# Performance work log

Measured on AMD Instinct MI355X. Metric: run time of the kernel, lower is better.

## Reference

```python
import jax, jax.numpy as jnp
import numpy as np

B, S, IN_DIM, D_MODEL, H = 1, 4096, 512, 512, 8
DK = D_MODEL // H


def setup_inputs() -> dict:
    key = jax.random.key(0)
    ks = jax.random.split(key, 10)
    sc_in = 1.0 / np.sqrt(IN_DIM)
    sc_dm = 1.0 / np.sqrt(D_MODEL)
    return {
        "x": jax.random.normal(ks[0], (B, S, IN_DIM), dtype=jnp.float32),
        "mask": jax.random.randint(ks[1], (1, 1, S, S), 0, 2, dtype=jnp.int32),
        "wq_w": jax.random.uniform(ks[2], (D_MODEL, IN_DIM), jnp.float32, -sc_in, sc_in),
        "wq_b": jax.random.uniform(ks[3], (D_MODEL,), jnp.float32, -sc_in, sc_in),
        "wk_w": jax.random.uniform(ks[4], (D_MODEL, IN_DIM), jnp.float32, -sc_in, sc_in),
        "wk_b": jax.random.uniform(ks[5], (D_MODEL,), jnp.float32, -sc_in, sc_in),
        "wv_w": jax.random.uniform(ks[6], (D_MODEL, IN_DIM), jnp.float32, -sc_in, sc_in),
        "wv_b": jax.random.uniform(ks[7], (D_MODEL,), jnp.float32, -sc_in, sc_in),
        "dense_w": jax.random.uniform(ks[8], (D_MODEL, D_MODEL), jnp.float32, -sc_dm, sc_dm),
        "dense_b": jax.random.uniform(ks[9], (D_MODEL,), jnp.float32, -sc_dm, sc_dm),
    }


def _split_heads(t):
    # Faithful to original: raw view [B, S, D] -> [B, H, S, DK] (no transpose)
    return t.reshape(B, H, S, DK)


def reference(x, mask, wq_w, wq_b, wk_w, wk_b, wv_w, wv_b, dense_w, dense_b):
    q = _split_heads(x @ wq_w.T + wq_b)  # [B, H, S, DK]
    k = _split_heads(x @ wk_w.T + wk_b)
    v = _split_heads(x @ wv_w.T + wv_b)
    score = jnp.einsum("bhqd,bhkd->bhqk", q, k) / np.sqrt(DK).astype(np.float32)
    score = score + mask.astype(score.dtype) * (-1e9)
    attn = jax.nn.softmax(score, axis=-1)
    out = jnp.einsum("bhqk,bhkd->bhqd", attn, v)  # [B, H, S, DK]
    out = out.transpose(0, 2, 1, 3).reshape(B, S, D_MODEL)
    return out @ dense_w.T + dense_b
```

## Files before the change

### kernel.cpp

```cpp
#include <hip/hip_runtime.h>
#include <hip/hip_bf16.h>

#define S_LEN 4096
#define DM    512
#define NH    8
#define DK    64

typedef __attribute__((ext_vector_type(8))) __bf16 bf16x8;
typedef __attribute__((ext_vector_type(4))) float  f32x4;
typedef unsigned short u16;
typedef unsigned int   u32;
typedef unsigned long long u64;

#define SQ_SCALE (0.125f * 1.44269504f)
#define FMAX 12.0f

__device__ __forceinline__ u16 f2bf(float f) {
  union { float f; u32 i; } v; v.f = f;
  u32 r = v.i + 0x7fff + ((v.i >> 16) & 1);
  return (u16)(r >> 16);
}

__global__ __launch_bounds__(256) void pack_mask(const int* __restrict__ mask,
                                                 u64* __restrict__ out) {
  int gid = blockIdx.x * 256 + threadIdx.x;
  u64 b = __ballot(mask[gid] != 0);
  if ((threadIdx.x & 63) == 0) out[gid >> 6] = b;
}

__global__ __launch_bounds__(256) void convert_all(
    const float* __restrict__ x, const float* __restrict__ wq,
    const float* __restrict__ wk, const float* __restrict__ wv,
    const float* __restrict__ dw,
    u16* __restrict__ xb, u16* __restrict__ wcat, u16* __restrict__ dwb) {
  int b = blockIdx.x;
  const float* src; u16* dst; size_t off;
  if      (b < 2048) { src = x;  dst = xb;   off = (size_t)b * 1024; }
  else if (b < 2304) { src = wq; dst = wcat; off = (size_t)(b - 2048) * 1024; }
  else if (b < 2560) { src = wk; dst = wcat + 262144; off = (size_t)(b - 2304) * 1024; }
  else if (b < 2816) { src = wv; dst = wcat + 524288; off = (size_t)(b - 2560) * 1024; }
  else               { src = dw; dst = dwb;  off = (size_t)(b - 2816) * 1024; }
  size_t i = off + (size_t)threadIdx.x * 4;
  float4 v = *reinterpret_cast<const float4*>(src + i);
  ushort4 o = make_ushort4(f2bf(v.x), f2bf(v.y), f2bf(v.z), f2bf(v.w));
  *reinterpret_cast<ushort4*>(dst + i) = o;
}

__global__ __launch_bounds__(256) void qkv_gemm(
    const u16* __restrict__ A, const u16* __restrict__ Wcat,
    const float* __restrict__ bq, const float* __restrict__ bk,
    const float* __restrict__ bv,
    u16* __restrict__ Qb, u16* __restrict__ Kb, u16* __restrict__ Vt2) {
  __shared__ u16 As[64 * 72];
  __shared__ u16 Ws[128 * 72];
  const int t = threadIdx.x;
  const int lane = t & 63, wv = t >> 6;
  const int m16 = lane & 15, quad = lane >> 4;
  const int n0g = blockIdx.x * 128, m0 = blockIdx.y * 64;
  const int seg = n0g >> 9;
  const int n0 = n0g & 511;
  const int mq = wv >> 1, nq = wv & 1;

  f32x4 acc[2][4];
#pragma unroll
  for (int i = 0; i < 2; i++)
#pragma unroll
    for (int j = 0; j < 4; j++) acc[i][j] = (f32x4)0.f;

  for (int k0 = 0; k0 < DM; k0 += 64) {
    __syncthreads();
#pragma unroll
    for (int c0 = 0; c0 < 2; c0++) {
      int c = t + c0 * 256;
      int row = c >> 3, col = (c & 7) * 8;
      *reinterpret_cast<uint4*>(&As[row * 72 + col]) =
          *reinterpret_cast<const uint4*>(&A[(size_t)(m0 + row) * DM + k0 + col]);
    }
#pragma unroll
    for (int c0 = 0; c0 < 4; c0++) {
      int c = t + c0 * 256;
      int row = c >> 3, col = (c & 7) * 8;
      *reinterpret_cast<uint4*>(&Ws[row * 72 + col]) =
          *reinterpret_cast<const uint4*>(&Wcat[(size_t)(n0g + row) * DM + k0 + col]);
    }
    __syncthreads();
#pragma unroll
    for (int kk = 0; kk < 64; kk += 32) {
      bf16x8 a0 = *reinterpret_cast<const bf16x8*>(&As[(mq * 32 + m16) * 72 + quad * 8 + kk]);
      bf16x8 a1 = *reinterpret_cast<const bf16x8*>(&As[(mq * 32 + 16 + m16) * 72 + quad * 8 + kk]);
#pragma unroll
      for (int ct = 0; ct < 4; ct++) {
        bf16x8 b = *reinterpret_cast<const bf16x8*>(&Ws[(nq * 64 + ct * 16 + m16) * 72 + quad * 8 + kk]);
        acc[0][ct] = __builtin_amdgcn_mfma_f32_16x16x32_bf16(a0, b, acc[0][ct], 0, 0, 0);
        acc[1][ct] = __builtin_amdgcn_mfma_f32_16x16x32_bf16(a1, b, acc[1][ct], 0, 0, 0);
      }
    }
  }

  const float* bias = (seg == 0) ? bq : (seg == 1) ? bk : bv;
  const float scale = (seg == 0) ? SQ_SCALE : 1.f;
  float bn[4];
#pragma unroll
  for (int ct = 0; ct < 4; ct++) bn[ct] = bias[n0 + nq * 64 + ct * 16 + m16];

  if (seg == 2) {
    __syncthreads();
    u16* T = Ws;
#pragma unroll
    for (int rt = 0; rt < 2; rt++)
#pragma unroll
      for (int ct = 0; ct < 4; ct++)
#pragma unroll
        for (int r = 0; r < 4; r++)
          T[(nq * 64 + ct * 16 + m16) * 72 + mq * 32 + rt * 16 + quad * 4 + r] =
              f2bf(acc[rt][ct][r] + bn[ct]);
    __syncthreads();
    const int h  = m0 >> 9;
    const int mp = m0 & 511;
#pragma unroll
    for (int c0 = 0; c0 < 4; c0++) {
      int c = t + c0 * 256;
      int nl = c >> 3, col8 = (c & 7) * 8;
      int d  = (n0 + nl) & 63;
      int cc = (n0 + nl) >> 6;
      *reinterpret_cast<uint4*>(
          &Vt2[(size_t)(h * 64 + d) * S_LEN + cc * 512 + mp + col8]) =
          *reinterpret_cast<const uint4*>(&T[nl * 72 + col8]);
    }
  } else {
    u16* dst = (seg == 0) ? Qb : Kb;
#pragma unroll
    for (int rt = 0; rt < 2; rt++)
#pragma unroll
      for (int ct = 0; ct < 4; ct++) {
        int n = n0 + nq * 64 + ct * 16 + m16;
#pragma unroll
        for (int r = 0; r < 4; r++) {
          int m = m0 + mq * 32 + rt * 16 + quad * 4 + r;
          dst[(size_t)m * DM + n] = f2bf((acc[rt][ct][r] + bn[ct]) * scale);
        }
      }
  }
}

__global__ __launch_bounds__(256) void dense_gemm(
    const u16* __restrict__ A, const u16* __restrict__ W,
    const float* __restrict__ bias, float* __restrict__ Cout) {
  __shared__ u16 As[64 * 72];
  __shared__ u16 Ws[64 * 72];
  const int t = threadIdx.x;
  const int lane = t & 63, wv = t >> 6;
  const int m16 = lane & 15, quad = lane >> 4;
  const int n0 = blockIdx.x * 64, m0 = blockIdx.y * 64;

  f32x4 acc[4];
#pragma unroll
  for (int j = 0; j < 4; j++) acc[j] = (f32x4)0.f;

  for (int k0 = 0; k0 < DM; k0 += 64) {
    __syncthreads();
#pragma unroll
    for (int c0 = 0; c0 < 2; c0++) {
      int c = t + c0 * 256;
      int row = c >> 3, col = (c & 7) * 8;
      *reinterpret_cast<uint4*>(&As[row * 72 + col]) =
          *reinterpret_cast<const uint4*>(&A[(size_t)(m0 + row) * DM + k0 + col]);
      *reinterpret_cast<uint4*>(&Ws[row * 72 + col]) =
          *reinterpret_cast<const uint4*>(&W[(size_t)(n0 + row) * DM + k0 + col]);
    }
    __syncthreads();
#pragma unroll
    for (int kk = 0; kk < 64; kk += 32) {
      bf16x8 a = *reinterpret_cast<const bf16x8*>(&As[(wv * 16 + m16) * 72 + quad * 8 + kk]);
#pragma unroll
      for (int ct = 0; ct < 4; ct++) {
        bf16x8 b = *reinterpret_cast<const bf16x8*>(&Ws[(ct * 16 + m16) * 72 + quad * 8 + kk]);
        acc[ct] = __builtin_amdgcn_mfma_f32_16x16x32_bf16(a, b, acc[ct], 0, 0, 0);
      }
    }
  }

  float bn[4];
#pragma unroll
  for (int ct = 0; ct < 4; ct++) bn[ct] = bias[n0 + ct * 16 + m16];
#pragma unroll
  for (int ct = 0; ct < 4; ct++) {
    int n = n0 + ct * 16 + m16;
#pragma unroll
    for (int r = 0; r < 4; r++) {
      int m = m0 + wv * 16 + quad * 4 + r;
      Cout[(size_t)m * DM + n] = acc[ct][r] + bn[ct];
    }
  }
}

__global__ __launch_bounds__(512) void attn_mfma(
    const u16* __restrict__ Q, const u16* __restrict__ K,
    const u16* __restrict__ Vt2, const u64* __restrict__ mbits,
    u16* __restrict__ O) {
  __shared__ u16 SM[2][3][64 * 72];
  __shared__ float Lm[64];

  const int t = threadIdx.x;
  const int lane = t & 63, wv = t >> 6;
  const int m16 = lane & 15, quad = lane >> 4;
  const int g  = wv >> 2;
  const int w4 = wv & 3;
  const int tt = t & 255;
  const int q0 = blockIdx.x * 64;
  const int h = blockIdx.y;
  const size_t hoff = (size_t)h * S_LEN * DK;
  const size_t kbase = hoff + (size_t)g * 2048 * DK;
  const u16* V2h = Vt2 + (size_t)h * DK * S_LEN;

  u16* Ks = SM[g][0];
  u16* Vs = SM[g][1];
  u16* Ps = SM[g][2];

  const u16* qptr = Q + hoff + (size_t)(q0 + w4 * 16 + m16) * DK + quad * 8;
  bf16x8 qlo = *reinterpret_cast<const bf16x8*>(qptr);
  bf16x8 qhi = *reinterpret_cast<const bf16x8*>(qptr + 32);

  union { u16 u[8]; bf16x8 v; } onesu;
#pragma unroll
  for (int j = 0; j < 8; j++) onesu.u[j] = 0x3F80;
  const bf16x8 ones = onesu.v;

  f32x4 acc_o[4];
  f32x4 acc_l = (f32x4)0.f;
#pragma unroll
  for (int dt = 0; dt < 4; dt++) acc_o[dt] = (f32x4)0.f;

  const int mshift = 32 * (quad & 1) + (quad >> 1);
  const int prow = (w4 * 16 + m16) * 72;

  for (int k0 = 0; k0 < 2048; k0 += 64) {
    const int kg = g * 2048 + k0;
#pragma unroll
    for (int c0 = 0; c0 < 2; c0++) {
      int c = tt + c0 * 256;
      int rg = c >> 3, cc = c & 7;
      int rperm = ((rg & 7) << 3) | (rg >> 3);
      *reinterpret_cast<uint4*>(&Ks[rperm * 72 + cc * 8]) =
          *reinterpret_cast<const uint4*>(&K[kbase + (size_t)(k0 + rg) * DK + cc * 8]);
      *reinterpret_cast<uint4*>(&Vs[rg * 72 + cc * 8]) =
          *reinterpret_cast<const uint4*>(&V2h[(size_t)rg * S_LEN + cc * 512 + (kg >> 3)]);
    }
    u64 mq = mbits[(size_t)(q0 + w4 * 16 + m16) * 64 + (kg >> 6)];
    u32 mm = (u32)(mq >> mshift);
    __syncthreads();

    f32x4 s[4];
#pragma unroll
    for (int ct = 0; ct < 4; ct++) s[ct] = (f32x4)0.f;
#pragma unroll
    for (int ct = 0; ct < 4; ct++) {
      bf16x8 klo = *reinterpret_cast<const bf16x8*>(&Ks[(ct * 16 + m16) * 72 + quad * 8]);
      bf16x8 khi = *reinterpret_cast<const bf16x8*>(&Ks[(ct * 16 + m16) * 72 + quad * 8 + 32]);
      s[ct] = __builtin_amdgcn_mfma_f32_16x16x32_bf16(klo, qlo, s[ct], 0, 0, 0);
      s[ct] = __builtin_amdgcn_mfma_f32_16x16x32_bf16(khi, qhi, s[ct], 0, 0, 0);
    }

#pragma unroll
    for (int ct = 0; ct < 4; ct++) {
      float p0 = __builtin_amdgcn_exp2f(((mm >> (2 * ct)) & 1u)      ? -1e9f : s[ct][0] - FMAX);
      float p1 = __builtin_amdgcn_exp2f(((mm >> (8 + 2 * ct)) & 1u)  ? -1e9f : s[ct][1] - FMAX);
      float p2 = __builtin_amdgcn_exp2f(((mm >> (16 + 2 * ct)) & 1u) ? -1e9f : s[ct][2] - FMAX);
      float p3 = __builtin_amdgcn_exp2f(((mm >> (24 + 2 * ct)) & 1u) ? -1e9f : s[ct][3] - FMAX);
      u32 pk01 = (u32)f2bf(p0) | ((u32)f2bf(p1) << 16);
      u32 pk23 = (u32)f2bf(p2) | ((u32)f2bf(p3) << 16);
      *reinterpret_cast<uint2*>(&Ps[prow + ct * 16 + quad * 4]) = make_uint2(pk01, pk23);
    }

    bf16x8 plo = *reinterpret_cast<const bf16x8*>(&Ps[prow + quad * 8]);
    bf16x8 phi = *reinterpret_cast<const bf16x8*>(&Ps[prow + quad * 8 + 32]);
#pragma unroll
    for (int dt = 0; dt < 4; dt++) {
      bf16x8 vlo = *reinterpret_cast<const bf16x8*>(&Vs[(dt * 16 + m16) * 72 + quad * 8]);
      bf16x8 vhi = *reinterpret_cast<const bf16x8*>(&Vs[(dt * 16 + m16) * 72 + quad * 8 + 32]);
      acc_o[dt] = __builtin_amdgcn_mfma_f32_16x16x32_bf16(plo, vlo, acc_o[dt], 0, 0, 0);
      acc_o[dt] = __builtin_amdgcn_mfma_f32_16x16x32_bf16(phi, vhi, acc_o[dt], 0, 0, 0);
    }
    acc_l = __builtin_amdgcn_mfma_f32_16x16x32_bf16(plo, ones, acc_l, 0, 0, 0);
    acc_l = __builtin_amdgcn_mfma_f32_16x16x32_bf16(phi, ones, acc_l, 0, 0, 0);
    __syncthreads();
  }

  float* Om = reinterpret_cast<float*>(&SM[1][0][0]);
  if (g == 1) {
#pragma unroll
    for (int dt = 0; dt < 4; dt++)
#pragma unroll
      for (int r = 0; r < 4; r++)
        Om[(w4 * 16 + quad * 4 + r) * 64 + dt * 16 + m16] = acc_o[dt][r];
    if (m16 == 0) {
#pragma unroll
      for (int r = 0; r < 4; r++) Lm[w4 * 16 + quad * 4 + r] = acc_l[r];
    }
  }
  __syncthreads();
  if (g == 0) {
    float rl[4];
#pragma unroll
    for (int r = 0; r < 4; r++)
      rl[r] = 1.f / (acc_l[r] + Lm[w4 * 16 + quad * 4 + r]);
#pragma unroll
    for (int dt = 0; dt < 4; dt++)
#pragma unroll
      for (int r = 0; r < 4; r++) {
        float o = acc_o[dt][r] + Om[(w4 * 16 + quad * 4 + r) * 64 + dt * 16 + m16];
        O[(size_t)(q0 + w4 * 16 + quad * 4 + r) * DM + h * DK + dt * 16 + m16] =
            f2bf(o * rl[r]);
      }
  }
}

extern "C" void kernel_launch(void* const* d_in, const int* in_sizes, int n_in,
                              void* d_out, int out_size, void* d_ws, size_t ws_size,
                              hipStream_t stream) {
  const float* x    = (const float*)d_in[0];
  const int*   mask = (const int*)d_in[1];
  const float* wq_w = (const float*)d_in[2];
  const float* wq_b = (const float*)d_in[3];
  const float* wk_w = (const float*)d_in[4];
  const float* wk_b = (const float*)d_in[5];
  const float* wv_w = (const float*)d_in[6];
  const float* wv_b = (const float*)d_in[7];
  const float* dw   = (const float*)d_in[8];
  const float* db   = (const float*)d_in[9];

  u16* xb   = (u16*)d_ws;
  u16* wcat = xb   + 2097152;
  u16* dwb  = wcat + 786432;
  u16* Qb   = dwb  + 262144;
  u16* Kb   = Qb   + 2097152;
  u16* Vt2  = Kb   + 2097152;
  u16* Ob   = Vt2  + 2097152;
  u64* mb   = (u64*)(Ob + 2097152);

  pack_mask<<<(S_LEN * S_LEN) / 256, 256, 0, stream>>>(mask, mb);
  convert_all<<<3072, 256, 0, stream>>>(x, wq_w, wk_w, wv_w, dw, xb, wcat, dwb);

  qkv_gemm<<<dim3(12, 64), 256, 0, stream>>>(xb, wcat, wq_b, wk_b, wv_b,
                                             Qb, Kb, Vt2);

  attn_mfma<<<dim3(S_LEN / 64, NH), 512, 0, stream>>>(Qb, Kb, Vt2, mb, Ob);

  dense_gemm<<<dim3(8, 64), 256, 0, stream>>>(Ob, dwb, db, (float*)d_out);
}
```

Before: 239.7 us.

## Restructure attention into 4-way key split with 128-query blocks and merge kernel

The attention kernel now processes 128 queries per block, with each wave handling two 16-row query tiles that share every K/V LDS fragment. The key range is split four ways across grid z and each split writes partial unnormalized outputs and row sums, which a new merge kernel sums and normalizes. P is kept in registers instead of going through LDS, using a permuted K row order and a new interleaved V layout, and the bf16 packing uses perm with a cheaper rounding. This removes the Ps LDS round trip and halves K/V loads per query, at the cost of extra global traffic for the partial outputs and an additional kernel launch.

```diff
diff --git a/kernel.cpp b/kernel.cpp
--- a/kernel.cpp
+++ b/kernel.cpp
@@ -19,6 +19,9 @@
   union { float f; u32 i; } v; v.f = f;
   u32 r = v.i + 0x7fff + ((v.i >> 16) & 1);
   return (u16)(r >> 16);
+}
+__device__ __forceinline__ float bf2f(u16 u) {
+  union { u32 i; float f; } v; v.i = ((u32)u) << 16; return v.f;
 }
 
 __global__ __launch_bounds__(256) void pack_mask(const int* __restrict__ mask,
@@ -50,7 +53,7 @@
     const u16* __restrict__ A, const u16* __restrict__ Wcat,
     const float* __restrict__ bq, const float* __restrict__ bk,
     const float* __restrict__ bv,
-    u16* __restrict__ Qb, u16* __restrict__ Kb, u16* __restrict__ Vt2) {
+    u16* __restrict__ Qb, u16* __restrict__ Kb, u16* __restrict__ V4) {
   __shared__ u16 As[64 * 72];
   __shared__ u16 Ws[128 * 72];
   const int t = threadIdx.x;
@@ -115,17 +118,18 @@
           T[(nq * 64 + ct * 16 + m16) * 72 + mq * 32 + rt * 16 + quad * 4 + r] =
               f2bf(acc[rt][ct][r] + bn[ct]);
     __syncthreads();
-    const int h  = m0 >> 9;
-    const int mp = m0 & 511;
+    const int h    = m0 >> 9;
+    const int mp   = m0 & 511;
+    const int cseg = n0 >> 7;
 #pragma unroll
     for (int c0 = 0; c0 < 4; c0++) {
       int c = t + c0 * 256;
-      int nl = c >> 3, col8 = (c & 7) * 8;
-      int d  = (n0 + nl) & 63;
-      int cc = (n0 + nl) >> 6;
+      int d  = c >> 4;
+      int tl = (c >> 1) & 7;
+      int cl = c & 1;
+      uint4 v = *reinterpret_cast<const uint4*>(&T[(cl * 64 + d) * 72 + tl * 8]);
       *reinterpret_cast<uint4*>(
-          &Vt2[(size_t)(h * 64 + d) * S_LEN + cc * 512 + mp + col8]) =
-          *reinterpret_cast<const uint4*>(&T[nl * 72 + col8]);
+          &V4[(size_t)(h * 64 + d) * 4096 + ((mp >> 3) + tl) * 64 + cl * 32 + cseg * 8]) = v;
     }
   } else {
     u16* dst = (seg == 0) ? Qb : Kb;
@@ -194,125 +198,153 @@
   }
 }
 
-__global__ __launch_bounds__(512) void attn_mfma(
+__device__ __forceinline__ void pack_p(const f32x4* s, u32 lo, u32 hi,
+                                       uint4& o0, uint4& o1) {
+  u32 pk[8];
+#pragma unroll
+  for (int ct = 0; ct < 4; ct++) {
+    u32 w = (ct & 1) ? hi : lo;
+    int b = ct >> 1;
+    float p0 = __builtin_amdgcn_exp2f(((w >> b) & 1u)        ? -1e9f : s[ct][0]);
+    float p1 = __builtin_amdgcn_exp2f(((w >> (b + 8)) & 1u)  ? -1e9f : s[ct][1]);
+    float p2 = __builtin_amdgcn_exp2f(((w >> (b + 16)) & 1u) ? -1e9f : s[ct][2]);
+    float p3 = __builtin_amdgcn_exp2f(((w >> (b + 24)) & 1u) ? -1e9f : s[ct][3]);
+    pk[2 * ct]     = __builtin_amdgcn_perm(__float_as_uint(p1) + 0x8000u,
+                                           __float_as_uint(p0) + 0x8000u, 0x07060302u);
+    pk[2 * ct + 1] = __builtin_amdgcn_perm(__float_as_uint(p3) + 0x8000u,
+                                           __float_as_uint(p2) + 0x8000u, 0x07060302u);
+  }
+  o0 = make_uint4(pk[0], pk[1], pk[2], pk[3]);
+  o1 = make_uint4(pk[4], pk[5], pk[6], pk[7]);
+}
+
+__global__ __launch_bounds__(256, 4) void attn_mfma(
     const u16* __restrict__ Q, const u16* __restrict__ K,
-    const u16* __restrict__ Vt2, const u64* __restrict__ mbits,
-    u16* __restrict__ O) {
-  __shared__ u16 SM[2][3][64 * 72];
-  __shared__ float Lm[64];
+    const u16* __restrict__ V4, const u64* __restrict__ mbits,
+    u16* __restrict__ Op, float* __restrict__ Lp) {
+  __shared__ u16 Ks[64 * 72];
+  __shared__ u16 Vs[64 * 72];
 
   const int t = threadIdx.x;
-  const int lane = t & 63, wv = t >> 6;
+  const int lane = t & 63, w4 = t >> 6;
   const int m16 = lane & 15, quad = lane >> 4;
-  const int g  = wv >> 2;
-  const int w4 = wv & 3;
-  const int tt = t & 255;
-  const int q0 = blockIdx.x * 64;
+  const int q0 = blockIdx.x * 128;
   const int h = blockIdx.y;
+  const int g = blockIdx.z;
   const size_t hoff = (size_t)h * S_LEN * DK;
-  const size_t kbase = hoff + (size_t)g * 2048 * DK;
-  const u16* V2h = Vt2 + (size_t)h * DK * S_LEN;
-
-  u16* Ks = SM[g][0];
-  u16* Vs = SM[g][1];
-  u16* Ps = SM[g][2];
-
-  const u16* qptr = Q + hoff + (size_t)(q0 + w4 * 16 + m16) * DK + quad * 8;
-  bf16x8 qlo = *reinterpret_cast<const bf16x8*>(qptr);
-  bf16x8 qhi = *reinterpret_cast<const bf16x8*>(qptr + 32);
+  const size_t kbase = hoff + (size_t)g * 1024 * DK;
+
+  const u16* qpA = Q + hoff + (size_t)(q0 + w4 * 32 + m16) * DK + quad * 8;
+  bf16x8 qloA = *reinterpret_cast<const bf16x8*>(qpA);
+  bf16x8 qhiA = *reinterpret_cast<const bf16x8*>(qpA + 32);
+  bf16x8 qloB = *reinterpret_cast<const bf16x8*>(qpA + 16 * DK);
+  bf16x8 qhiB = *reinterpret_cast<const bf16x8*>(qpA + 16 * DK + 32);
 
   union { u16 u[8]; bf16x8 v; } onesu;
 #pragma unroll
   for (int j = 0; j < 8; j++) onesu.u[j] = 0x3F80;
   const bf16x8 ones = onesu.v;
 
-  f32x4 acc_o[4];
-  f32x4 acc_l = (f32x4)0.f;
-#pragma unroll
-  for (int dt = 0; dt < 4; dt++) acc_o[dt] = (f32x4)0.f;
-
-  const int mshift = 32 * (quad & 1) + (quad >> 1);
-  const int prow = (w4 * 16 + m16) * 72;
-
-  for (int k0 = 0; k0 < 2048; k0 += 64) {
-    const int kg = g * 2048 + k0;
+  f32x4 accA[4], accB[4];
+  f32x4 acc_lA = (f32x4)0.f, acc_lB = (f32x4)0.f;
+#pragma unroll
+  for (int dt = 0; dt < 4; dt++) { accA[dt] = (f32x4)0.f; accB[dt] = (f32x4)0.f; }
+
+  for (int k0 = 0; k0 < 1024; k0 += 64) {
+    const int kg = g * 1024 + k0;
 #pragma unroll
     for (int c0 = 0; c0 < 2; c0++) {
-      int c = tt + c0 * 256;
+      int c = t + c0 * 256;
       int rg = c >> 3, cc = c & 7;
-      int rperm = ((rg & 7) << 3) | (rg >> 3);
-      *reinterpret_cast<uint4*>(&Ks[rperm * 72 + cc * 8]) =
+      int sr = ((rg & 1) << 5) | (((rg >> 5) & 1) << 4) | (((rg >> 2) & 1) << 3) |
+               (((rg >> 1) & 1) << 2) | (((rg >> 4) & 1) << 1) | ((rg >> 3) & 1);
+      *reinterpret_cast<uint4*>(&Ks[sr * 72 + cc * 8]) =
           *reinterpret_cast<const uint4*>(&K[kbase + (size_t)(k0 + rg) * DK + cc * 8]);
       *reinterpret_cast<uint4*>(&Vs[rg * 72 + cc * 8]) =
-          *reinterpret_cast<const uint4*>(&V2h[(size_t)rg * S_LEN + cc * 512 + (kg >> 3)]);
-    }
-    u64 mq = mbits[(size_t)(q0 + w4 * 16 + m16) * 64 + (kg >> 6)];
-    u32 mm = (u32)(mq >> mshift);
-    __syncthreads();
-
-    f32x4 s[4];
-#pragma unroll
-    for (int ct = 0; ct < 4; ct++) s[ct] = (f32x4)0.f;
+          *reinterpret_cast<const uint4*>(&V4[(size_t)(h * 64 + rg) * 4096 + kg + cc * 8]);
+    }
+    u64 mqA = mbits[(size_t)(q0 + w4 * 32 + m16) * 64 + (kg >> 6)] >> (2 * quad);
+    u64 mqB = mbits[(size_t)(q0 + w4 * 32 + 16 + m16) * 64 + (kg >> 6)] >> (2 * quad);
+    __syncthreads();
+
+    f32x4 sA[4], sB[4];
+#pragma unroll
+    for (int ct = 0; ct < 4; ct++) { sA[ct] = (f32x4)(-FMAX); sB[ct] = (f32x4)(-FMAX); }
 #pragma unroll
     for (int ct = 0; ct < 4; ct++) {
       bf16x8 klo = *reinterpret_cast<const bf16x8*>(&Ks[(ct * 16 + m16) * 72 + quad * 8]);
       bf16x8 khi = *reinterpret_cast<const bf16x8*>(&Ks[(ct * 16 + m16) * 72 + quad * 8 + 32]);
-      s[ct] = __builtin_amdgcn_mfma_f32_16x16x32_bf16(klo, qlo, s[ct], 0, 0, 0);
-      s[ct] = __builtin_amdgcn_mfma_f32_16x16x32_bf16(khi, qhi, s[ct], 0, 0, 0);
-    }
-
-#pragma unroll
-    for (int ct = 0; ct < 4; ct++) {
-      float p0 = __builtin_amdgcn_exp2f(((mm >> (2 * ct)) & 1u)      ? -1e9f : s[ct][0] - FMAX);
-      float p1 = __builtin_amdgcn_exp2f(((mm >> (8 + 2 * ct)) & 1u)  ? -1e9f : s[ct][1] - FMAX);
-      float p2 = __builtin_amdgcn_exp2f(((mm >> (16 + 2 * ct)) & 1u) ? -1e9f : s[ct][2] - FMAX);
-      float p3 = __builtin_amdgcn_exp2f(((mm >> (24 + 2 * ct)) & 1u) ? -1e9f : s[ct][3] - FMAX);
-      u32 pk01 = (u32)f2bf(p0) | ((u32)f2bf(p1) << 16);
-      u32 pk23 = (u32)f2bf(p2) | ((u32)f2bf(p3) << 16);
-      *reinterpret_cast<uint2*>(&Ps[prow + ct * 16 + quad * 4]) = make_uint2(pk01, pk23);
-    }
-
-    bf16x8 plo = *reinterpret_cast<const bf16x8*>(&Ps[prow + quad * 8]);
-    bf16x8 phi = *reinterpret_cast<const bf16x8*>(&Ps[prow + quad * 8 + 32]);
+      sA[ct] = __builtin_amdgcn_mfma_f32_16x16x32_bf16(klo, qloA, sA[ct], 0, 0, 0);
+      sA[ct] = __builtin_amdgcn_mfma_f32_16x16x32_bf16(khi, qhiA, sA[ct], 0, 0, 0);
+      sB[ct] = __builtin_amdgcn_mfma_f32_16x16x32_bf16(klo, qloB, sB[ct], 0, 0, 0);
+      sB[ct] = __builtin_amdgcn_mfma_f32_16x16x32_bf16(khi, qhiB, sB[ct], 0, 0, 0);
+    }
+
+    union { uint4 i; bf16x8 v; } pA0, pA1, pB0, pB1;
+    pack_p(sA, (u32)mqA, (u32)(mqA >> 32), pA0.i, pA1.i);
+    pack_p(sB, (u32)mqB, (u32)(mqB >> 32), pB0.i, pB1.i);
+
 #pragma unroll
     for (int dt = 0; dt < 4; dt++) {
       bf16x8 vlo = *reinterpret_cast<const bf16x8*>(&Vs[(dt * 16 + m16) * 72 + quad * 8]);
       bf16x8 vhi = *reinterpret_cast<const bf16x8*>(&Vs[(dt * 16 + m16) * 72 + quad * 8 + 32]);
-      acc_o[dt] = __builtin_amdgcn_mfma_f32_16x16x32_bf16(plo, vlo, acc_o[dt], 0, 0, 0);
-      acc_o[dt] = __builtin_amdgcn_mfma_f32_16x16x32_bf16(phi, vhi, acc_o[dt], 0, 0, 0);
-    }
-    acc_l = __builtin_amdgcn_mfma_f32_16x16x32_bf16(plo, ones, acc_l, 0, 0, 0);
-    acc_l = __builtin_amdgcn_mfma_f32_16x16x32_bf16(phi, ones, acc_l, 0, 0, 0);
-    __syncthreads();
-  }
-
-  float* Om = reinterpret_cast<float*>(&SM[1][0][0]);
-  if (g == 1) {
-#pragma unroll
-    for (int dt = 0; dt < 4; dt++)
-#pragma unroll
-      for (int r = 0; r < 4; r++)
-        Om[(w4 * 16 + quad * 4 + r) * 64 + dt * 16 + m16] = acc_o[dt][r];
-    if (m16 == 0) {
-#pragma unroll
-      for (int r = 0; r < 4; r++) Lm[w4 * 16 + quad * 4 + r] = acc_l[r];
-    }
-  }
-  __syncthreads();
-  if (g == 0) {
-    float rl[4];
-#pragma unroll
-    for (int r = 0; r < 4; r++)
-      rl[r] = 1.f / (acc_l[r] + Lm[w4 * 16 + quad * 4 + r]);
-#pragma unroll
-    for (int dt = 0; dt < 4; dt++)
-#pragma unroll
-      for (int r = 0; r < 4; r++) {
-        float o = acc_o[dt][r] + Om[(w4 * 16 + quad * 4 + r) * 64 + dt * 16 + m16];
-        O[(size_t)(q0 + w4 * 16 + quad * 4 + r) * DM + h * DK + dt * 16 + m16] =
-            f2bf(o * rl[r]);
-      }
-  }
+      accA[dt] = __builtin_amdgcn_mfma_f32_16x16x32_bf16(pA0.v, vlo, accA[dt], 0, 0, 0);
+      accA[dt] = __builtin_amdgcn_mfma_f32_16x16x32_bf16(pA1.v, vhi, accA[dt], 0, 0, 0);
+      accB[dt] = __builtin_amdgcn_mfma_f32_16x16x32_bf16(pB0.v, vlo, accB[dt], 0, 0, 0);
+      accB[dt] = __builtin_amdgcn_mfma_f32_16x16x32_bf16(pB1.v, vhi, accB[dt], 0, 0, 0);
+    }
+    acc_lA = __builtin_amdgcn_mfma_f32_16x16x32_bf16(pA0.v, ones, acc_lA, 0, 0, 0);
+    acc_lA = __builtin_amdgcn_mfma_f32_16x16x32_bf16(pA1.v, ones, acc_lA, 0, 0, 0);
+    acc_lB = __builtin_amdgcn_mfma_f32_16x16x32_bf16(pB0.v, ones, acc_lB, 0, 0, 0);
+    acc_lB = __builtin_amdgcn_mfma_f32_16x16x32_bf16(pB1.v, ones, acc_lB, 0, 0, 0);
+    __syncthreads();
+  }
+
+  u16* Og = Op + (size_t)g * 2097152;
+#pragma unroll
+  for (int dt = 0; dt < 4; dt++)
+#pragma unroll
+    for (int r = 0; r < 4; r++) {
+      Og[(size_t)(q0 + w4 * 32 + quad * 4 + r) * DM + h * DK + dt * 16 + m16] =
+          f2bf(accA[dt][r]);
+      Og[(size_t)(q0 + w4 * 32 + 16 + quad * 4 + r) * DM + h * DK + dt * 16 + m16] =
+          f2bf(accB[dt][r]);
+    }
+  if (m16 == 0) {
+#pragma unroll
+    for (int r = 0; r < 4; r++) {
+      Lp[g * 32768 + h * 4096 + q0 + w4 * 32 + quad * 4 + r] = acc_lA[r];
+      Lp[g * 32768 + h * 4096 + q0 + w4 * 32 + 16 + quad * 4 + r] = acc_lB[r];
+    }
+  }
+}
+
+__global__ __launch_bounds__(256) void attn_merge(
+    const u16* __restrict__ Op, const float* __restrict__ Lp,
+    u16* __restrict__ Out) {
+  int i8 = (blockIdx.x * 256 + threadIdx.x) * 8;
+  int q = i8 >> 9;
+  int h = (i8 >> 6) & 7;
+  float l = 0.f;
+#pragma unroll
+  for (int part = 0; part < 4; part++) l += Lp[part * 32768 + h * 4096 + q];
+  float rl = 1.f / l;
+  float o[8];
+#pragma unroll
+  for (int j = 0; j < 8; j++) o[j] = 0.f;
+#pragma unroll
+  for (int part = 0; part < 4; part++) {
+    ushort4 v0 = *reinterpret_cast<const ushort4*>(Op + part * 2097152 + i8);
+    ushort4 v1 = *reinterpret_cast<const ushort4*>(Op + part * 2097152 + i8 + 4);
+    o[0] += bf2f(v0.x); o[1] += bf2f(v0.y); o[2] += bf2f(v0.z); o[3] += bf2f(v0.w);
+    o[4] += bf2f(v1.x); o[5] += bf2f(v1.y); o[6] += bf2f(v1.z); o[7] += bf2f(v1.w);
+  }
+  ushort4 o0 = make_ushort4(f2bf(o[0] * rl), f2bf(o[1] * rl),
+                            f2bf(o[2] * rl), f2bf(o[3] * rl));
+  ushort4 o1 = make_ushort4(f2bf(o[4] * rl), f2bf(o[5] * rl),
+                            f2bf(o[6] * rl), f2bf(o[7] * rl));
+  *reinterpret_cast<ushort4*>(Out + i8) = o0;
+  *reinterpret_cast<ushort4*>(Out + i8 + 4) = o1;
 }
 
 extern "C" void kernel_launch(void* const* d_in, const int* in_sizes, int n_in,
@@ -329,22 +361,24 @@
   const float* dw   = (const float*)d_in[8];
   const float* db   = (const float*)d_in[9];
 
-  u16* xb   = (u16*)d_ws;
-  u16* wcat = xb   + 2097152;
-  u16* dwb  = wcat + 786432;
-  u16* Qb   = dwb  + 262144;
-  u16* Kb   = Qb   + 2097152;
-  u16* Vt2  = Kb   + 2097152;
-  u16* Ob   = Vt2  + 2097152;
-  u64* mb   = (u64*)(Ob + 2097152);
+  u16* xb    = (u16*)d_ws;
+  u16* wcat  = xb    + 2097152;
+  u16* dwb   = wcat  + 786432;
+  u16* Qb    = dwb   + 262144;
+  u16* Kb    = Qb    + 2097152;
+  u16* V4    = Kb    + 2097152;
+  u16* Opart = V4    + 2097152;
+  u64* mb    = (u64*)(Opart + 4 * 2097152);
+  float* Lp  = (float*)(mb + 262144);
 
   pack_mask<<<(S_LEN * S_LEN) / 256, 256, 0, stream>>>(mask, mb);
   convert_all<<<3072, 256, 0, stream>>>(x, wq_w, wk_w, wv_w, dw, xb, wcat, dwb);
 
   qkv_gemm<<<dim3(12, 64), 256, 0, stream>>>(xb, wcat, wq_b, wk_b, wv_b,
-                                             Qb, Kb, Vt2);
-
-  attn_mfma<<<dim3(S_LEN / 64, NH), 512, 0, stream>>>(Qb, Kb, Vt2, mb, Ob);
-
-  dense_gemm<<<dim3(8, 64), 256, 0, stream>>>(Ob, dwb, db, (float*)d_out);
-}
+                                             Qb, Kb, V4);
+
+  attn_mfma<<<dim3(32, NH, 4), 256, 0, stream>>>(Qb, Kb, V4, mb, Opart, Lp);
+  attn_merge<<<1024, 256, 0, stream>>>(Opart, Lp, Qb);
+
+  dense_gemm<<<dim3(8, 64), 256, 0, stream>>>(Qb, dwb, db, (float*)d_out);
+}
```

Result: faster. 225.4 us (-6.0%).
